# Kernel optimization log

Hardware: AMD Instinct MI355X
Metric: run time of the kernel (lower is better)

The kernel has to match this reference:

```python
import jax, jax.numpy as jnp
import numpy as np

ROT_DIM = 32
THETA = 10000.0
HEAD_SIZE = 192


def _rope(t):
    # t: [B, T, D]; rotate first ROT_DIM features with interleaved-pair RoPE
    T = t.shape[1]
    inv_freq = 1.0 / (THETA ** (jnp.arange(0, ROT_DIM, 2, dtype=jnp.float32) / ROT_DIM))  # [16]
    freqs = jnp.arange(T, dtype=jnp.float32)[:, None] * inv_freq[None, :]  # [T,16]
    freqs = jnp.repeat(freqs, 2, axis=-1)  # [T,32], each freq repeated for the pair
    cos = jnp.cos(freqs).astype(t.dtype)
    sin = jnp.sin(freqs).astype(t.dtype)
    x = t[..., :ROT_DIM]
    x1 = x[..., 0::2]
    x2 = x[..., 1::2]
    rot_half = jnp.stack([-x2, x1], axis=-1).reshape(x.shape)  # interleave (-x2, x1)
    rotated = x * cos + rot_half * sin
    return jnp.concatenate([rotated, t[..., ROT_DIM:]], axis=-1)


def setup_inputs() -> dict:
    key = jax.random.key(0)
    k1, k2, k3, k4 = jax.random.split(key, 4)
    B, T, C, H = 64, 512, 768, HEAD_SIZE
    x = jax.random.normal(k1, (B, T, C), dtype=jnp.float32)
    s = 1.0 / np.sqrt(C)
    Wq = jax.random.normal(k2, (C, H), dtype=jnp.float32) * s
    Wk = jax.random.normal(k3, (C, H), dtype=jnp.float32) * s
    Wv = jax.random.normal(k4, (C, H), dtype=jnp.float32) * s
    return {"x": x, "Wq": Wq, "Wk": Wk, "Wv": Wv}


def reference(x, Wq, Wk, Wv):
    B, T, C = x.shape
    q = x @ Wq  # [B,T,H]
    k = x @ Wk
    v = x @ Wv
    q = _rope(q)
    k = _rope(k)
    scale = k.shape[-1] ** -0.5
    scores = jnp.einsum('bqh,bkh->bqk', q, k) * scale  # [B,T,T]
    causal = jnp.tril(jnp.ones((T, T), dtype=bool))
    scores = jnp.where(causal[None, :, :], scores, -jnp.inf)
    weight = jax.nn.softmax(scores, axis=-1)
    # dropout is identity at eval time
    out = jnp.einsum('bqk,bkh->bqh', weight, v)  # [B,T,H]
    return out
```

## Files before the change

kernel.cpp:

```cpp
#include <hip/hip_runtime.h>
#include <cstdint>

typedef __attribute__((ext_vector_type(8))) short short8;
typedef __attribute__((ext_vector_type(4))) float floatx4;

__device__ __forceinline__ unsigned short f2bf(float f) {
  uint32_t u = __builtin_bit_cast(uint32_t, f);
  u += 0x7fffu + ((u >> 16) & 1u);
  return (unsigned short)(u >> 16);
}
__device__ __forceinline__ uint32_t pkbf(float lo, float hi) {
  uint32_t a = __builtin_bit_cast(uint32_t, lo) + 0x8000u;
  uint32_t b = __builtin_bit_cast(uint32_t, hi) + 0x8000u;
  return __builtin_amdgcn_perm(b, a, 0x07060302);
}
__device__ __forceinline__ void gll16(const void* g, void* l) {
  __builtin_amdgcn_global_load_lds(
      (const __attribute__((address_space(1))) unsigned int*)g,
      (__attribute__((address_space(3))) unsigned int*)l, 16, 0, 0);
}

__global__ void prep_w_kernel(const float* __restrict__ Wq,
                              const float* __restrict__ Wk,
                              const float* __restrict__ Wv,
                              unsigned short* __restrict__ Wt) {
  int id = blockIdx.x * 256 + threadIdx.x;
  int bz = id / 18432, rem = id - bz * 18432;
  int kb = rem / 768, s = rem - kb * 768;
  int row = s >> 2, cs = s & 3;
  int c = cs ^ ((row >> 1) & 3);
  const float* W = (bz == 0) ? Wq : (bz == 1) ? Wk : Wv;
  int k0 = kb * 32 + c * 8;
  unsigned short v[8];
#pragma unroll
  for (int e = 0; e < 8; ++e) v[e] = f2bf(W[(size_t)(k0 + e) * 192 + row]);
  uint4 o;
  o.x = v[0] | ((uint32_t)v[1] << 16);
  o.y = v[2] | ((uint32_t)v[3] << 16);
  o.z = v[4] | ((uint32_t)v[5] << 16);
  o.w = v[6] | ((uint32_t)v[7] << 16);
  *(uint4*)(Wt + (size_t)id * 8) = o;
}

__global__ __launch_bounds__(256, 2) void proj_kernel(
    const float* __restrict__ x, const unsigned short* __restrict__ Wt,
    unsigned short* __restrict__ q_ws, unsigned short* __restrict__ k_ws,
    unsigned short* __restrict__ v_ws) {
  __shared__ __align__(16) unsigned short A_lds[3][128 * 32];
  __shared__ __align__(16) unsigned short B_lds[3][192 * 32];
  const int tid = threadIdx.x;
  const int w = tid >> 6, l = tid & 63, quad = l >> 4, ln = l & 15;
  const int m0 = blockIdx.x * 128;
  const int bz = blockIdx.y;

  const int arow = tid >> 2, ac = tid & 3;
  const int aslot = ((ac ^ ((arow >> 1) & 3)) << 4);
  const float* xp0 = x + (size_t)(m0 + arow) * 768 + ac * 8;
  const float* xp1 = xp0 + (size_t)64 * 768;
  const unsigned short* wimg = Wt + (size_t)bz * 18432 * 8;

  const int fq = ((quad ^ ((ln >> 1) & 3)) << 4);

  floatx4 acc[2][12];
#pragma unroll
  for (int mi = 0; mi < 2; ++mi)
#pragma unroll
    for (int nj = 0; nj < 12; ++nj) acc[mi][nj] = floatx4{0.f, 0.f, 0.f, 0.f};

  float4 a0p, a0q, a0r, a0s, a1p, a1q, a1r, a1s, a2p, a2q, a2r, a2s;

#define LOADA(S, K0)                               \
  do {                                             \
    a##S##p = *(const float4*)(xp0 + (K0));        \
    a##S##q = *(const float4*)(xp0 + (K0) + 4);    \
    a##S##r = *(const float4*)(xp1 + (K0));        \
    a##S##s = *(const float4*)(xp1 + (K0) + 4);    \
  } while (0)
#define STAGEA(S, AB)                                                   \
  do {                                                                  \
    uint4 ap;                                                           \
    ap.x = pkbf(a##S##p.x, a##S##p.y);                                  \
    ap.y = pkbf(a##S##p.z, a##S##p.w);                                  \
    ap.z = pkbf(a##S##q.x, a##S##q.y);                                  \
    ap.w = pkbf(a##S##q.z, a##S##q.w);                                  \
    *(uint4*)((char*)&A_lds[AB][0] + arow * 64 + aslot) = ap;           \
    ap.x = pkbf(a##S##r.x, a##S##r.y);                                  \
    ap.y = pkbf(a##S##r.z, a##S##r.w);                                  \
    ap.z = pkbf(a##S##s.x, a##S##s.y);                                  \
    ap.w = pkbf(a##S##s.z, a##S##s.w);                                  \
    *(uint4*)((char*)&A_lds[AB][0] + (arow + 64) * 64 + aslot) = ap;    \
  } while (0)
#define DMAB(KB1, BB)                                             \
  do {                                                            \
    const unsigned short* src = wimg + (size_t)(KB1)*6144;        \
    char* dstb = (char*)&B_lds[BB][0];                            \
    gll16(src + tid * 8, dstb + tid * 16);                        \
    gll16(src + (256 + tid) * 8, dstb + (256 + tid) * 16);        \
    gll16(src + (512 + tid) * 8, dstb + (512 + tid) * 16);        \
  } while (0)
#define WAITBAR(N)                                                          \
  asm volatile("s_waitcnt vmcnt(" #N ") lgkmcnt(0)\n\ts_barrier" ::: "memory")
#define PCOMPUTE(C)                                                              \
  do {                                                                           \
    short8 af0 = *(const short8*)((const char*)&A_lds[C][0] +                    \
                                  (w * 32 + ln) * 64 + fq);                      \
    short8 af1 = *(const short8*)((const char*)&A_lds[C][0] +                    \
                                  (w * 32 + 16 + ln) * 64 + fq);                 \
    _Pragma("unroll") for (int nj = 0; nj < 12; ++nj) {                          \
      short8 bf = *(const short8*)((const char*)&B_lds[C][0] +                   \
                                   (nj * 16 + ln) * 64 + fq);                    \
      acc[0][nj] = __builtin_amdgcn_mfma_f32_16x16x32_bf16(af0, bf, acc[0][nj],  \
                                                           0, 0, 0);             \
      acc[1][nj] = __builtin_amdgcn_mfma_f32_16x16x32_bf16(af1, bf, acc[1][nj],  \
                                                           0, 0, 0);             \
    }                                                                            \
  } while (0)
#define BODY(KB, C, P)            \
  do {                            \
    STAGEA(P, P);                 \
    DMAB((KB) + 1, P);            \
    LOADA(C, ((KB) + 3) * 32);    \
    WAITBAR(7);                   \
    PCOMPUTE(C);                  \
  } while (0)

  DMAB(0, 0);
  LOADA(0, 0);
  LOADA(1, 32);
  LOADA(2, 64);
  STAGEA(0, 0);

  BODY(0, 0, 1);
  for (int t = 1; t <= 16; t += 3) {
    BODY(t, 1, 2);
    BODY(t + 1, 2, 0);
    BODY(t + 2, 0, 1);
  }
  BODY(19, 1, 2);
  BODY(20, 2, 0);
  { STAGEA(1, 1); DMAB(22, 1); WAITBAR(3); PCOMPUTE(0); }
  { STAGEA(2, 2); DMAB(23, 2); WAITBAR(3); PCOMPUTE(1); }
  { WAITBAR(0); PCOMPUTE(2); }
#undef LOADA
#undef STAGEA
#undef DMAB
#undef WAITBAR
#undef PCOMPUTE
#undef BODY

  const float R_LG = 0.8304820237218406f;
  if (bz < 2) {
    unsigned short* dst = (bz == 0) ? q_ws : k_ws;
#pragma unroll
    for (int mi = 0; mi < 2; ++mi)
#pragma unroll
      for (int r = 0; r < 4; ++r) {
        int row_g = m0 + w * 32 + mi * 16 + quad * 4 + r;
        int t_pos = row_g & 511;
        float v0 = acc[mi][0][r], v1 = acc[mi][1][r];
        {
          float i0 = (float)(ln >> 1);
          float f0 = exp2f(-i0 * R_LG);
          float f1 = exp2f(-(i0 + 8.0f) * R_LG);
          float s0, c0, s1, c1;
          sincosf((float)t_pos * f0, &s0, &c0);
          sincosf((float)t_pos * f1, &s1, &c1);
          float p0 = __shfl_xor(v0, 1), p1 = __shfl_xor(v1, 1);
          v0 = (ln & 1) ? (v0 * c0 + p0 * s0) : (v0 * c0 - p0 * s0);
          v1 = (ln & 1) ? (v1 * c1 + p1 * s1) : (v1 * c1 - p1 * s1);
        }
        dst[(size_t)row_g * 192 + ln] = f2bf(v0);
        dst[(size_t)row_g * 192 + 16 + ln] = f2bf(v1);
#pragma unroll
        for (int nj = 2; nj < 12; ++nj)
          dst[(size_t)row_g * 192 + nj * 16 + ln] = f2bf(acc[mi][nj][r]);
      }
  } else {
#pragma unroll
    for (int mi = 0; mi < 2; ++mi) {
      int rb = m0 + w * 32 + mi * 16 + quad * 4;
      int bb = rb >> 9, t = rb & 511;
#pragma unroll
      for (int nj = 0; nj < 12; ++nj) {
        ushort4 pv;
        pv.x = f2bf(acc[mi][nj][0]);
        pv.y = f2bf(acc[mi][nj][1]);
        pv.z = f2bf(acc[mi][nj][2]);
        pv.w = f2bf(acc[mi][nj][3]);
        *(ushort4*)&v_ws[((size_t)bb * 192 + nj * 16 + ln) * 512 + t] = pv;
      }
    }
  }
}

__global__ __launch_bounds__(256) void attn_kernel(
    const unsigned short* __restrict__ q_ws, const unsigned short* __restrict__ k_ws,
    const unsigned short* __restrict__ v_ws, float* __restrict__ out) {
  __shared__ __align__(16) unsigned short K_lds[32 * 200];
  __shared__ __align__(16) unsigned short V_lds[192 * 40];
  __shared__ __align__(16) unsigned short P_lds[4][16 * 40];
  const int tid = threadIdx.x;
  const int w = tid >> 6, l = tid & 63, quad = l >> 4, ln = l & 15;
  const int b = blockIdx.y;
  const int qt = (blockIdx.y < 32) ? blockIdx.x : 7 - blockIdx.x;
  const int q0 = qt * 64;

  short8 qf[6];
  {
    const unsigned short* qp =
        q_ws + (size_t)(b * 512 + q0 + w * 16 + ln) * 192 + quad * 8;
#pragma unroll
    for (int kk = 0; kk < 6; ++kk) qf[kk] = *(const short8*)(qp + kk * 32);
  }

  float m_i[4], l_i[4];
  floatx4 o[12];
#pragma unroll
  for (int r = 0; r < 4; ++r) { m_i[r] = -1e30f; l_i[r] = 0.f; }
#pragma unroll
  for (int nt = 0; nt < 12; ++nt) o[nt] = floatx4{0.f, 0.f, 0.f, 0.f};
  const float sm_scale = 0.07216878364870323f;

  const int ktmax = 2 * qt + 1;
  for (int kt = 0; kt <= ktmax; ++kt) {
    const int k0 = kt * 32;
    __syncthreads();
#pragma unroll
    for (int it = 0; it < 3; ++it) {
      int idx = it * 256 + tid;
      int row = idx / 24, c = idx - row * 24;
      uint4 v = *(const uint4*)(k_ws + (size_t)(b * 512 + k0 + row) * 192 + c * 8);
      *(uint4*)&K_lds[row * 200 + c * 8] = v;
    }
#pragma unroll
    for (int it = 0; it < 3; ++it) {
      int idx = it * 256 + tid;
      int row = idx >> 2, c = idx & 3;
      uint4 v = *(const uint4*)(v_ws + (size_t)(b * 192 + row) * 512 + k0 + c * 8);
      *(uint4*)&V_lds[row * 40 + c * 8] = v;
    }
    __syncthreads();

    float s[2][4];
    __builtin_amdgcn_s_setprio(1);
#pragma unroll
    for (int nt = 0; nt < 2; ++nt) {
      floatx4 sa = floatx4{0.f, 0.f, 0.f, 0.f};
#pragma unroll
      for (int kk = 0; kk < 6; ++kk) {
        short8 kf = *(const short8*)&K_lds[(nt * 16 + ln) * 200 + kk * 32 + quad * 8];
        sa = __builtin_amdgcn_mfma_f32_16x16x32_bf16(qf[kk], kf, sa, 0, 0, 0);
      }
#pragma unroll
      for (int r = 0; r < 4; ++r) s[nt][r] = sa[r] * sm_scale;
    }
    __builtin_amdgcn_s_setprio(0);
    if (kt >= 2 * qt) {
      int kd = (kt - 2 * qt) * 32;
#pragma unroll
      for (int nt = 0; nt < 2; ++nt)
#pragma unroll
        for (int r = 0; r < 4; ++r)
          if (kd + nt * 16 + ln > w * 16 + quad * 4 + r) s[nt][r] = -1e30f;
    }
    float alpha[4];
#pragma unroll
    for (int r = 0; r < 4; ++r) {
      float mx = fmaxf(s[0][r], s[1][r]);
      mx = fmaxf(mx, __shfl_xor(mx, 1));
      mx = fmaxf(mx, __shfl_xor(mx, 2));
      mx = fmaxf(mx, __shfl_xor(mx, 4));
      mx = fmaxf(mx, __shfl_xor(mx, 8));
      float mnew = fmaxf(m_i[r], mx);
      alpha[r] = __expf(m_i[r] - mnew);
      float sum = 0.f;
#pragma unroll
      for (int nt = 0; nt < 2; ++nt) {
        s[nt][r] = __expf(s[nt][r] - mnew);
        sum += s[nt][r];
      }
      sum += __shfl_xor(sum, 1);
      sum += __shfl_xor(sum, 2);
      sum += __shfl_xor(sum, 4);
      sum += __shfl_xor(sum, 8);
      l_i[r] = l_i[r] * alpha[r] + sum;
      m_i[r] = mnew;
    }
#pragma unroll
    for (int nt = 0; nt < 12; ++nt)
#pragma unroll
      for (int r = 0; r < 4; ++r) o[nt][r] *= alpha[r];

#pragma unroll
    for (int nt = 0; nt < 2; ++nt)
#pragma unroll
      for (int r = 0; r < 4; ++r)
        P_lds[w][(quad * 4 + r) * 40 + nt * 16 + ln] = f2bf(s[nt][r]);
    __asm__ volatile("s_waitcnt lgkmcnt(0)" ::: "memory");

    __builtin_amdgcn_s_setprio(1);
    {
      short8 pf = *(const short8*)&P_lds[w][ln * 40 + quad * 8];
#pragma unroll
      for (int nt = 0; nt < 12; ++nt) {
        short8 vf = *(const short8*)&V_lds[(nt * 16 + ln) * 40 + quad * 8];
        o[nt] = __builtin_amdgcn_mfma_f32_16x16x32_bf16(pf, vf, o[nt], 0, 0, 0);
      }
    }
    __builtin_amdgcn_s_setprio(0);
  }

#pragma unroll
  for (int r = 0; r < 4; ++r) {
    float inv = 1.0f / l_i[r];
    size_t rowoff = (size_t)(b * 512 + q0 + w * 16 + quad * 4 + r) * 192;
#pragma unroll
    for (int nt = 0; nt < 12; ++nt)
      out[rowoff + nt * 16 + ln] = o[nt][r] * inv;
  }
}

extern "C" void kernel_launch(void* const* d_in, const int* in_sizes, int n_in,
                              void* d_out, int out_size, void* d_ws, size_t ws_size,
                              hipStream_t stream) {
  const float* x = (const float*)d_in[0];
  const float* Wq = (const float*)d_in[1];
  const float* Wk = (const float*)d_in[2];
  const float* Wv = (const float*)d_in[3];
  float* out = (float*)d_out;

  char* ws = (char*)d_ws;
  const size_t QKV_BYTES = (size_t)64 * 512 * 192 * 2;
  unsigned short* q_ws = (unsigned short*)(ws);
  unsigned short* k_ws = (unsigned short*)(ws + QKV_BYTES);
  unsigned short* v_ws = (unsigned short*)(ws + 2 * QKV_BYTES);
  unsigned short* Wt = (unsigned short*)(ws + 3 * QKV_BYTES);

  hipLaunchKernelGGL(prep_w_kernel, dim3(216), dim3(256), 0, stream, Wq, Wk, Wv, Wt);
  hipLaunchKernelGGL(proj_kernel, dim3(256, 3), dim3(256), 0, stream, x, Wt, q_ws, k_ws, v_ws);
  hipLaunchKernelGGL(attn_kernel, dim3(8, 64), dim3(256), 0, stream, q_ws, k_ws, v_ws, out);
}
```

Before: 234.6 us.

## Stream fp32 x tiles into LDS via async DMA and convert at fragment load

```diff
diff --git a/kernel.cpp b/kernel.cpp
--- a/kernel.cpp
+++ b/kernel.cpp
@@ -46,20 +46,21 @@
     const float* __restrict__ x, const unsigned short* __restrict__ Wt,
     unsigned short* __restrict__ q_ws, unsigned short* __restrict__ k_ws,
     unsigned short* __restrict__ v_ws) {
-  __shared__ __align__(16) unsigned short A_lds[3][128 * 32];
-  __shared__ __align__(16) unsigned short B_lds[3][192 * 32];
+  __shared__ __align__(16) float A_lds[3][128 * 32];
+  __shared__ __align__(16) unsigned short B_lds[2][192 * 32];
   const int tid = threadIdx.x;
   const int w = tid >> 6, l = tid & 63, quad = l >> 4, ln = l & 15;
   const int m0 = blockIdx.x * 128;
   const int bz = blockIdx.y;
 
-  const int arow = tid >> 2, ac = tid & 3;
-  const int aslot = ((ac ^ ((arow >> 1) & 3)) << 4);
-  const float* xp0 = x + (size_t)(m0 + arow) * 768 + ac * 8;
-  const float* xp1 = xp0 + (size_t)64 * 768;
+  const int arow7 = (tid >> 3) & 7;
+  const int aswz = (tid & 7) ^ arow7;
+  const float* xsrc = x + (size_t)(m0 + (tid >> 3)) * 768 + aswz * 4;
   const unsigned short* wimg = Wt + (size_t)bz * 18432 * 8;
 
   const int fq = ((quad ^ ((ln >> 1) & 3)) << 4);
+  const int as0 = ((2 * quad) ^ (ln & 7)) << 4;
+  const int as1 = as0 ^ 16;
 
   floatx4 acc[2][12];
 #pragma unroll
@@ -67,32 +68,16 @@
 #pragma unroll
     for (int nj = 0; nj < 12; ++nj) acc[mi][nj] = floatx4{0.f, 0.f, 0.f, 0.f};
 
-  float4 a0p, a0q, a0r, a0s, a1p, a1q, a1r, a1s, a2p, a2q, a2r, a2s;
-
-#define LOADA(S, K0)                               \
-  do {                                             \
-    a##S##p = *(const float4*)(xp0 + (K0));        \
-    a##S##q = *(const float4*)(xp0 + (K0) + 4);    \
-    a##S##r = *(const float4*)(xp1 + (K0));        \
-    a##S##s = *(const float4*)(xp1 + (K0) + 4);    \
-  } while (0)
-#define STAGEA(S, AB)                                                   \
+#define DMAA(KB, AB)                                                    \
   do {                                                                  \
-    uint4 ap;                                                           \
-    ap.x = pkbf(a##S##p.x, a##S##p.y);                                  \
-    ap.y = pkbf(a##S##p.z, a##S##p.w);                                  \
-    ap.z = pkbf(a##S##q.x, a##S##q.y);                                  \
-    ap.w = pkbf(a##S##q.z, a##S##q.w);                                  \
-    *(uint4*)((char*)&A_lds[AB][0] + arow * 64 + aslot) = ap;           \
-    ap.x = pkbf(a##S##r.x, a##S##r.y);                                  \
-    ap.y = pkbf(a##S##r.z, a##S##r.w);                                  \
-    ap.z = pkbf(a##S##s.x, a##S##s.y);                                  \
-    ap.w = pkbf(a##S##s.z, a##S##s.w);                                  \
-    *(uint4*)((char*)&A_lds[AB][0] + (arow + 64) * 64 + aslot) = ap;    \
-  } while (0)
-#define DMAB(KB1, BB)                                             \
+    char* dsta = (char*)&A_lds[AB][0];                                  \
+    _Pragma("unroll") for (int it = 0; it < 4; ++it)                    \
+        gll16(xsrc + (size_t)it * 32 * 768 + (KB) * 32,                 \
+              dsta + (it * 256 + tid) * 16);                            \
+  } while (0)
+#define DMAB(KB, BB)                                              \
   do {                                                            \
-    const unsigned short* src = wimg + (size_t)(KB1)*6144;        \
+    const unsigned short* src = wimg + (size_t)(KB)*6144;         \
     char* dstb = (char*)&B_lds[BB][0];                            \
     gll16(src + tid * 8, dstb + tid * 16);                        \
     gll16(src + (256 + tid) * 8, dstb + (256 + tid) * 16);        \
@@ -100,14 +85,22 @@
   } while (0)
 #define WAITBAR(N)                                                          \
   asm volatile("s_waitcnt vmcnt(" #N ") lgkmcnt(0)\n\ts_barrier" ::: "memory")
-#define PCOMPUTE(C)                                                              \
+#define AFRAG(DST, CA, ROWB)                                                  \
+  short8 DST;                                                                 \
+  do {                                                                        \
+    const char* ab = (const char*)&A_lds[CA][0] + (ROWB) * 128;               \
+    float4 c0 = *(const float4*)(ab + as0);                                   \
+    float4 c1 = *(const float4*)(ab + as1);                                   \
+    uint4 u = {pkbf(c0.x, c0.y), pkbf(c0.z, c0.w),                            \
+               pkbf(c1.x, c1.y), pkbf(c1.z, c1.w)};                           \
+    DST = __builtin_bit_cast(short8, u);                                      \
+  } while (0)
+#define PCOMPUTE(CA, CB)                                                         \
   do {                                                                           \
-    short8 af0 = *(const short8*)((const char*)&A_lds[C][0] +                    \
-                                  (w * 32 + ln) * 64 + fq);                      \
-    short8 af1 = *(const short8*)((const char*)&A_lds[C][0] +                    \
-                                  (w * 32 + 16 + ln) * 64 + fq);                 \
+    AFRAG(af0, CA, w * 32 + ln);                                                 \
+    AFRAG(af1, CA, w * 32 + 16 + ln);                                            \
     _Pragma("unroll") for (int nj = 0; nj < 12; ++nj) {                          \
-      short8 bf = *(const short8*)((const char*)&B_lds[C][0] +                   \
+      short8 bf = *(const short8*)((const char*)&B_lds[CB][0] +                  \
                                    (nj * 16 + ln) * 64 + fq);                    \
       acc[0][nj] = __builtin_amdgcn_mfma_f32_16x16x32_bf16(af0, bf, acc[0][nj],  \
                                                            0, 0, 0);             \
@@ -115,36 +108,36 @@
                                                            0, 0, 0);             \
     }                                                                            \
   } while (0)
-#define BODY(KB, C, P)            \
+#define BODY(J, AN, BN, CA, CB)   \
   do {                            \
-    STAGEA(P, P);                 \
-    DMAB((KB) + 1, P);            \
-    LOADA(C, ((KB) + 3) * 32);    \
-    WAITBAR(7);                   \
-    PCOMPUTE(C);                  \
+    WAITBAR(4);                   \
+    DMAB((J) + 1, BN);            \
+    DMAA((J) + 2, AN);            \
+    PCOMPUTE(CA, CB);             \
   } while (0)
 
   DMAB(0, 0);
-  LOADA(0, 0);
-  LOADA(1, 32);
-  LOADA(2, 64);
-  STAGEA(0, 0);
-
-  BODY(0, 0, 1);
-  for (int t = 1; t <= 16; t += 3) {
-    BODY(t, 1, 2);
-    BODY(t + 1, 2, 0);
-    BODY(t + 2, 0, 1);
-  }
-  BODY(19, 1, 2);
-  BODY(20, 2, 0);
-  { STAGEA(1, 1); DMAB(22, 1); WAITBAR(3); PCOMPUTE(0); }
-  { STAGEA(2, 2); DMAB(23, 2); WAITBAR(3); PCOMPUTE(1); }
-  { WAITBAR(0); PCOMPUTE(2); }
-#undef LOADA
-#undef STAGEA
+  DMAA(0, 0);
+  DMAA(1, 1);
+
+  for (int t = 0; t < 18; t += 6) {
+    BODY(t + 0, 2, 1, 0, 0);
+    BODY(t + 1, 0, 0, 1, 1);
+    BODY(t + 2, 1, 1, 2, 0);
+    BODY(t + 3, 2, 0, 0, 1);
+    BODY(t + 4, 0, 1, 1, 0);
+    BODY(t + 5, 1, 0, 2, 1);
+  }
+  BODY(18, 2, 1, 0, 0);
+  BODY(19, 0, 0, 1, 1);
+  BODY(20, 1, 1, 2, 0);
+  BODY(21, 2, 0, 0, 1);
+  { WAITBAR(4); DMAB(23, 1); PCOMPUTE(1, 0); }
+  { WAITBAR(0); PCOMPUTE(2, 1); }
+#undef DMAA
 #undef DMAB
 #undef WAITBAR
+#undef AFRAG
 #undef PCOMPUTE
 #undef BODY
 
```

Measured after the change: 235.7 us. No clear change (+0.5%).
